# Kernel tuning notes

Measured on AMD Instinct MI355X. Metric: run time of the kernel, lower is better.

Reference implementation:

```python
import jax, jax.numpy as jnp
from jax import lax
import numpy as np

HID = 64      # lstm hidden / gat in-dim
HEADS = 4
DH = HID // HEADS  # 16 per-head dim
OUT = 3       # horizon


def setup_inputs() -> dict:
    key = jax.random.key(0)
    ks = jax.random.split(key, 18)
    B, T, N = 8, 12, 1500
    p = lambda k, shape: jax.random.normal(k, shape, jnp.float32) * 0.1
    return {
        "x": jax.random.normal(ks[0], (B, T, N), jnp.float32),
        "adj": jax.random.randint(ks[1], (N, N), 0, 2, jnp.int32),
        "lstm_Wih0": p(ks[2], (4 * HID, 1)),
        "lstm_Whh0": p(ks[3], (4 * HID, HID)),
        "lstm_bih0": p(ks[4], (4 * HID,)),
        "lstm_bhh0": p(ks[5], (4 * HID,)),
        "lstm_Wih1": p(ks[6], (4 * HID, HID)),
        "lstm_Whh1": p(ks[7], (4 * HID, HID)),
        "lstm_bih1": p(ks[8], (4 * HID,)),
        "lstm_bhh1": p(ks[9], (4 * HID,)),
        "gat0_W": p(ks[10], (HID, HID)),
        "gat0_asrc": p(ks[11], (HEADS, DH)),
        "gat0_adst": p(ks[12], (HEADS, DH)),
        "gat1_W": p(ks[13], (HID, HID)),
        "gat1_asrc": p(ks[14], (HEADS, DH)),
        "gat1_adst": p(ks[15], (HEADS, DH)),
        "out_W": p(ks[16], (OUT, HID)),
        "out_b": p(ks[17], (OUT,)),
    }


def _lstm_layer(seq, Wih, Whh, bih, bhh):
    # seq: (T, BN, in) -> (T, BN, H). PyTorch gate order i,f,g,o.
    BN = seq.shape[1]
    H = Whh.shape[1]

    def step(carry, xt):
        h, c = carry
        g = xt @ Wih.T + h @ Whh.T + bih + bhh
        i, f, gg, o = jnp.split(g, 4, axis=-1)
        c = jax.nn.sigmoid(f) * c + jax.nn.sigmoid(i) * jnp.tanh(gg)
        h = jax.nn.sigmoid(o) * jnp.tanh(c)
        return (h, c), h

    zero = jnp.zeros((BN, H), seq.dtype)
    _, hs = lax.scan(step, (zero, zero), seq)
    return hs


def _gat(h_in, W, asrc, adst, mask):
    # h_in: (B,N,HID); mask: (1,N,N,1) bool
    B, N, _ = h_in.shape
    Hn, D = asrc.shape
    hp = (h_in @ W.T).reshape(B, N, Hn, D)           # (B,N,H,D)
    e_src = jnp.einsum('bnhd,hd->bnh', hp, asrc)
    e_dst = jnp.einsum('bnhd,hd->bnh', hp, adst)
    e = e_src[:, :, None, :] + e_dst[:, None, :, :]   # (B,i,j,H)
    e = jnp.where(e > 0, e, 0.2 * e)                  # LeakyReLU(0.2)
    e = jnp.where(mask, e, -jnp.inf)
    alpha = jax.nn.softmax(e, axis=2)                 # softmax over neighbors j
    ho = jnp.einsum('bijh,bjhd->bihd', alpha, hp)
    return ho.reshape(B, N, Hn * D)


def reference(x, adj, lstm_Wih0, lstm_Whh0, lstm_bih0, lstm_bhh0,
              lstm_Wih1, lstm_Whh1, lstm_bih1, lstm_bhh1,
              gat0_W, gat0_asrc, gat0_adst, gat1_W, gat1_asrc, gat1_adst,
              out_W, out_b):
    B, T, N = x.shape
    # (B,T,N) -> (B*N, T, 1) -> time-major (T, B*N, 1)
    xf = jnp.transpose(x, (0, 2, 1)).reshape(B * N, T, 1)
    seq = jnp.transpose(xf, (1, 0, 2))
    hs = _lstm_layer(seq, lstm_Wih0, lstm_Whh0, lstm_bih0, lstm_bhh0)
    hs = _lstm_layer(hs, lstm_Wih1, lstm_Whh1, lstm_bih1, lstm_bhh1)
    h = hs[-1].reshape(B, N, HID)                     # last-step hidden of top layer
    mask = (adj > 0)[None, :, :, None]
    h = jax.nn.relu(_gat(h, gat0_W, gat0_asrc, gat0_adst, mask))
    h = jax.nn.relu(_gat(h, gat1_W, gat1_asrc, gat1_adst, mask))
    out = h @ out_W.T + out_b                         # (B,N,OUT)
    return jnp.transpose(out, (0, 2, 1))              # (B,OUT,N)
```

## Files before the change

kernel.cpp:

```cpp
#include <hip/hip_runtime.h>
#include <hip/hip_bf16.h>


#define BN 12000
#define NNODE 1500
#define NB 8
#define TT 12
#define NPAD 1536
#define LOG2E 1.44269504f

typedef __bf16 bf16x8 __attribute__((ext_vector_type(8)));
typedef __bf16 bf16x4 __attribute__((ext_vector_type(4)));
typedef float  f32x4  __attribute__((ext_vector_type(4)));

__device__ __forceinline__ float rcpf(float v) { return __builtin_amdgcn_rcpf(v); }
__device__ __forceinline__ float exp2f_(float v) { return __builtin_amdgcn_exp2f(v); }
__device__ __forceinline__ float sigf(float v) { return rcpf(1.f + __expf(-v)); }
__device__ __forceinline__ float tanhf_(float v) {
    return fmaf(2.f, rcpf(1.f + __expf(-2.f * v)), -1.f);
}

__device__ __forceinline__ bf16x8 ldcvt(const float* p) {
    f32x4 a = *(const f32x4*)p;
    f32x4 b = *(const f32x4*)(p + 4);
    bf16x8 r;
    #pragma unroll
    for (int i = 0; i < 4; ++i) { r[i] = (__bf16)a[i]; r[4 + i] = (__bf16)b[i]; }
    return r;
}

__global__ __launch_bounds__(512, 1) void lstm_mask_prep(
    const float* __restrict__ x,
    const float* __restrict__ Wih0, const float* __restrict__ Whh0,
    const float* __restrict__ bih0, const float* __restrict__ bhh0,
    const float* __restrict__ Wih1, const float* __restrict__ Whh1,
    const float* __restrict__ bih1, const float* __restrict__ bhh1,
    const int* __restrict__ adj, unsigned int* __restrict__ mask,
    const float* __restrict__ gW, const float* __restrict__ asrc,
    const float* __restrict__ adst,
    __bf16* __restrict__ hpT, float* __restrict__ esT, float* __restrict__ edT)
{
    if (blockIdx.x >= 750) {
        int wid  = (blockIdx.x - 750) * 8 + (threadIdx.x >> 6);
        int lane = threadIdx.x & 63;
        #pragma unroll 4
        for (int u = 0; u < 16; ++u) {
            int task = wid * 16 + u;
            int i = task / 24, ch = task - i * 24;
            int j = ch * 64 + lane;
            int a = (i < NNODE && j < NNODE) ? adj[i * NNODE + j] : 0;
            unsigned long long m = __ballot(a > 0);
            if (lane == 0 && i < 1504) *(unsigned long long*)&mask[i * 48 + ch * 2] = m;
        }
        return;
    }

    __shared__ __align__(16) __bf16 h0s[16 * 72];
    __shared__ __align__(16) __bf16 h1s[16 * 72];
    __shared__ __align__(16) float  xls[TT * 16];
    __shared__ float avs[128];
    __shared__ __align__(16) __bf16 hp_t[64 * 24];

    int tid  = threadIdx.x;
    int w    = __builtin_amdgcn_readfirstlane(tid >> 6);
    int lane = tid & 63;
    int l15  = lane & 15;
    int qd   = lane >> 4;
    bool lo  = l15 < 8;
    int dloc = l15 & 7;
    int d    = 8 * w + dloc;

    for (int e = tid; e < (16 * 72) / 2; e += 512) ((unsigned int*)h1s)[e] = 0u;
    if (tid < TT * 16) {
        int t = tid >> 4, m = tid & 15;
        int s = blockIdx.x * 16 + m;
        int bb = s / NNODE, nn = s - bb * NNODE;
        xls[tid] = x[bb * (TT * NNODE) + t * NNODE + nn];
    }
    if (tid < 64)       avs[tid] = asrc[tid] * LOG2E;
    else if (tid < 128) avs[tid] = adst[tid - 64] * LOG2E;

    int gA = (lo ? 0 : 64) + d;
    int gB = (lo ? 128 : 192) + d;
    bf16x8 B0A[2], B0B[2], B1A[4], B1B[4];
    #pragma unroll
    for (int kt = 0; kt < 2; ++kt) {
        B0A[kt] = ldcvt(&Whh0[gA * 64 + 32 * kt + 8 * qd]);
        B0B[kt] = ldcvt(&Whh0[gB * 64 + 32 * kt + 8 * qd]);
        B1A[kt] = ldcvt(&Wih1[gA * 64 + 32 * kt + 8 * qd]);
        B1B[kt] = ldcvt(&Wih1[gB * 64 + 32 * kt + 8 * qd]);
        B1A[kt + 2] = ldcvt(&Whh1[gA * 64 + 32 * kt + 8 * qd]);
        B1B[kt + 2] = ldcvt(&Whh1[gB * 64 + 32 * kt + 8 * qd]);
    }
    float b0A = bih0[gA] + bhh0[gA], b0B = bih0[gB] + bhh0[gB];
    float b1A = bih1[gA] + bhh1[gA], b1B = bih1[gB] + bhh1[gB];
    float w0A = Wih0[gA], w0B = Wih0[gB];

    float pwi = Wih0[d],       pbi = bih0[d]       + bhh0[d];
    float pwg = Wih0[128 + d], pbg = bih0[128 + d] + bhh0[128 + d];
    float pwo = Wih0[192 + d], pbo = bih0[192 + d] + bhh0[192 + d];

    float c0[2], c1[2];
    c0[0] = c0[1] = c1[0] = c1[1] = 0.f;

    __syncthreads();

    #pragma unroll
    for (int rl = 0; rl < 2; ++rl) {
        int rr = lo ? rl : 2 + rl;
        int m = 4 * qd + rr;
        float xv = xls[m];
        float gi = fmaf(pwi, xv, pbi);
        float gg = fmaf(pwg, xv, pbg);
        float go = fmaf(pwo, xv, pbo);
        float c = sigf(gi) * tanhf_(gg);
        c0[rl] = c;
        h0s[m * 72 + d] = (__bf16)(sigf(go) * tanhf_(c));
    }
    __syncthreads();

    for (int t = 0; t < TT; ++t) {
        bool last = (t == TT - 1);
        bf16x8 a0[2], a1[2];
        #pragma unroll
        for (int kt = 0; kt < 2; ++kt) {
            a0[kt] = *(bf16x8*)&h0s[l15 * 72 + 32 * kt + 8 * qd];
            a1[kt] = *(bf16x8*)&h1s[l15 * 72 + 32 * kt + 8 * qd];
        }
        f32x4 AA1, AB1, AA0, AB0;
        #pragma unroll
        for (int r = 0; r < 4; ++r) { AA1[r] = b1A; AB1[r] = b1B; }
        if (!last) {
            f32x4 xv = *(f32x4*)&xls[(t + 1) * 16 + 4 * qd];
            #pragma unroll
            for (int r = 0; r < 4; ++r) {
                AA0[r] = fmaf(w0A, xv[r], b0A);
                AB0[r] = fmaf(w0B, xv[r], b0B);
            }
        }
        #pragma unroll
        for (int kt = 0; kt < 2; ++kt) {
            AA1 = __builtin_amdgcn_mfma_f32_16x16x32_bf16(a0[kt], B1A[kt], AA1, 0, 0, 0);
            AB1 = __builtin_amdgcn_mfma_f32_16x16x32_bf16(a0[kt], B1B[kt], AB1, 0, 0, 0);
            AA1 = __builtin_amdgcn_mfma_f32_16x16x32_bf16(a1[kt], B1A[kt + 2], AA1, 0, 0, 0);
            AB1 = __builtin_amdgcn_mfma_f32_16x16x32_bf16(a1[kt], B1B[kt + 2], AB1, 0, 0, 0);
        }
        if (!last) {
            #pragma unroll
            for (int kt = 0; kt < 2; ++kt) {
                AA0 = __builtin_amdgcn_mfma_f32_16x16x32_bf16(a0[kt], B0A[kt], AA0, 0, 0, 0);
                AB0 = __builtin_amdgcn_mfma_f32_16x16x32_bf16(a0[kt], B0B[kt], AB0, 0, 0, 0);
            }
        }
        __syncthreads();

        {
            float shA0 = __shfl_xor(lo ? AA1[2] : AA1[0], 8);
            float shA1 = __shfl_xor(lo ? AA1[3] : AA1[1], 8);
            float shB0 = __shfl_xor(lo ? AB1[2] : AB1[0], 8);
            float shB1 = __shfl_xor(lo ? AB1[3] : AB1[1], 8);
            #pragma unroll
            for (int rl = 0; rl < 2; ++rl) {
                int rr = lo ? rl : 2 + rl;
                float ownA = AA1[rr], ownB = AB1[rr];
                float shA = rl ? shA1 : shA0, shB = rl ? shB1 : shB0;
                float gi = lo ? ownA : shA;
                float gf = lo ? shA : ownA;
                float gg = lo ? ownB : shB;
                float go = lo ? shB : ownB;
                float c = sigf(gf) * c1[rl] + sigf(gi) * tanhf_(gg);
                c1[rl] = c;
                float hv = sigf(go) * tanhf_(c);
                int m = 4 * qd + rr;
                h1s[m * 72 + d] = (__bf16)hv;
            }
        }
        if (!last) {
            float shA0 = __shfl_xor(lo ? AA0[2] : AA0[0], 8);
            float shA1 = __shfl_xor(lo ? AA0[3] : AA0[1], 8);
            float shB0 = __shfl_xor(lo ? AB0[2] : AB0[0], 8);
            float shB1 = __shfl_xor(lo ? AB0[3] : AB0[1], 8);
            #pragma unroll
            for (int rl = 0; rl < 2; ++rl) {
                int rr = lo ? rl : 2 + rl;
                float ownA = AA0[rr], ownB = AB0[rr];
                float shA = rl ? shA1 : shA0, shB = rl ? shB1 : shB0;
                float gi = lo ? ownA : shA;
                float gf = lo ? shA : ownA;
                float gg = lo ? ownB : shB;
                float go = lo ? shB : ownB;
                float c = sigf(gf) * c0[rl] + sigf(gi) * tanhf_(gg);
                c0[rl] = c;
                int m = 4 * qd + rr;
                h0s[m * 72 + d] = (__bf16)(sigf(go) * tanhf_(c));
            }
        }
        __syncthreads();
    }

    int s0 = blockIdx.x * 16;
    if (w < 4) {
        int mt = w;
        bf16x8 Bf0 = *(bf16x8*)&h1s[l15 * 72 + 8 * qd];
        bf16x8 Bf1 = *(bf16x8*)&h1s[l15 * 72 + 32 + 8 * qd];
        bf16x8 A0 = ldcvt(&gW[(mt * 16 + l15) * 64 + 8 * qd]);
        bf16x8 A1 = ldcvt(&gW[(mt * 16 + l15) * 64 + 32 + 8 * qd]);
        f32x4 a = {0.f, 0.f, 0.f, 0.f};
        a = __builtin_amdgcn_mfma_f32_16x16x32_bf16(A0, Bf0, a, 0, 0, 0);
        a = __builtin_amdgcn_mfma_f32_16x16x32_bf16(A1, Bf1, a, 0, 0, 0);
        float ts = 0.f, td = 0.f;
        #pragma unroll
        for (int r = 0; r < 4; ++r) {
            int dd = mt * 16 + qd * 4 + r;
            ts = fmaf(a[r], avs[dd], ts);
            td = fmaf(a[r], avs[64 + dd], td);
            hp_t[dd * 24 + l15] = (__bf16)a[r];
        }
        ts += __shfl_xor(ts, 16); ts += __shfl_xor(ts, 32);
        td += __shfl_xor(td, 16); td += __shfl_xor(td, 32);
        if (qd == 0) {
            int s = s0 + l15, b = s / NNODE, n = s - b * NNODE;
            esT[(b * 4 + mt) * NPAD + n] = ts;
            edT[(b * 4 + mt) * NPAD + n] = td;
        }
    }
    __syncthreads();
    if (tid < 256) {
        int dim = tid >> 2, seg = tid & 3;
        int b0 = s0 / NNODE, b1 = (s0 + 15) / NNODE;
        if (b0 == b1) {
            int n0 = s0 - b0 * NNODE;
            bf16x4 v = *(bf16x4*)&hp_t[dim * 24 + seg * 4];
            *(bf16x4*)&hpT[((b0 << 6) + dim) * NPAD + n0 + seg * 4] = v;
        } else {
            #pragma unroll
            for (int u = 0; u < 4; ++u) {
                int ss = s0 + seg * 4 + u;
                int b = ss / NNODE, n = ss - b * NNODE;
                hpT[((b << 6) + dim) * NPAD + n] = hp_t[dim * 24 + seg * 4 + u];
            }
        }
    }
}

__global__ __launch_bounds__(512, 1) void gat_mid(
    const __bf16* __restrict__ hpT, const float* __restrict__ esT,
    const float* __restrict__ edT, const unsigned int* __restrict__ mask,
    const float* __restrict__ gW, const float* __restrict__ asrc,
    const float* __restrict__ adst,
    __bf16* __restrict__ hpT1, float* __restrict__ esT1, float* __restrict__ edT1)
{
    __shared__ float Ss[8][16];
    __shared__ float hbuf[32 * 72];
    __shared__ float avs[128];
    __shared__ __align__(16) __bf16 hp1_t[64 * 40];

    int tid  = threadIdx.x;
    int wv   = tid >> 6;
    int lane = tid & 63;
    int l15  = lane & 15;
    int qd   = lane >> 4;
    int hh   = wv & 3;
    int ig   = wv >> 2;
    int b    = blockIdx.x / 47;
    int i0   = (blockIdx.x % 47) * 32;
    int it   = i0 + ig * 16;

    if (tid < 64)       avs[tid] = asrc[tid] * LOG2E;
    else if (tid < 128) avs[tid] = adst[tid - 64] * LOG2E;

    const __bf16* Brow = hpT + (((b << 6) + (hh << 4) + l15) * NPAD);
    const float* edrow = edT + (b * 4 + hh) * NPAD;
    const unsigned int* mrow = mask + (it + l15) * 48;
    float esv = esT[(b * 4 + hh) * NPAD + it + l15];

    f32x4 acc = {0.f, 0.f, 0.f, 0.f};
    float S = 0.f;

    for (int jt = 0; jt < 12; ++jt) {
        uint4 mw = *(const uint4*)&mrow[jt * 4];
        #pragma unroll
        for (int kt = 0; kt < 4; ++kt) {
            int jk = jt * 128 + kt * 32 + qd * 8;
            float4 e0 = *(const float4*)&edrow[jk];
            float4 e1 = *(const float4*)&edrow[jk + 4];
            unsigned int mb = ((&mw.x)[kt] >> (qd * 8)) & 0xffu;
            float ej[8] = {e0.x, e0.y, e0.z, e0.w, e1.x, e1.y, e1.z, e1.w};
            bf16x8 A;
            #pragma unroll
            for (int jj = 0; jj < 8; ++jj) {
                float e = esv + ej[jj];
                e = fmaxf(e, 0.2f * e);
                float p = ((mb >> jj) & 1u) ? exp2f_(e) : 0.f;
                S += p;
                A[jj] = (__bf16)p;
            }
            bf16x8 B = *(const bf16x8*)&Brow[jk];
            acc = __builtin_amdgcn_mfma_f32_16x16x32_bf16(A, B, acc, 0, 0, 0);
        }
    }

    S += __shfl_xor(S, 16);
    S += __shfl_xor(S, 32);
    if (qd == 0) Ss[wv][l15] = S;
    __syncthreads();

    #pragma unroll
    for (int r = 0; r < 4; ++r) {
        float rs = rcpf(Ss[wv][qd * 4 + r]);
        hbuf[(ig * 16 + qd * 4 + r) * 72 + (hh << 4) + l15] = fmaxf(acc[r] * rs, 0.f);
    }
    __syncthreads();

    {
        int mt = hh;
        bf16x8 Bf0 = ldcvt(&hbuf[(ig * 16 + l15) * 72 + 8 * qd]);
        bf16x8 Bf1 = ldcvt(&hbuf[(ig * 16 + l15) * 72 + 32 + 8 * qd]);
        bf16x8 A0 = ldcvt(&gW[(mt * 16 + l15) * 64 + 8 * qd]);
        bf16x8 A1 = ldcvt(&gW[(mt * 16 + l15) * 64 + 32 + 8 * qd]);
        f32x4 a = {0.f, 0.f, 0.f, 0.f};
        a = __builtin_amdgcn_mfma_f32_16x16x32_bf16(A0, Bf0, a, 0, 0, 0);
        a = __builtin_amdgcn_mfma_f32_16x16x32_bf16(A1, Bf1, a, 0, 0, 0);
        float ts = 0.f, td = 0.f;
        #pragma unroll
        for (int r = 0; r < 4; ++r) {
            int dd = mt * 16 + qd * 4 + r;
            ts = fmaf(a[r], avs[dd], ts);
            td = fmaf(a[r], avs[64 + dd], td);
            hp1_t[dd * 40 + ig * 16 + l15] = (__bf16)a[r];
        }
        ts += __shfl_xor(ts, 16); ts += __shfl_xor(ts, 32);
        td += __shfl_xor(td, 16); td += __shfl_xor(td, 32);
        if (qd == 0) {
            int n = i0 + ig * 16 + l15;
            esT1[(b * 4 + mt) * NPAD + n] = ts;
            edT1[(b * 4 + mt) * NPAD + n] = td;
        }
    }
    __syncthreads();
    if (tid < 256) {
        int dim = tid >> 2, seg = tid & 3;
        bf16x8 v = *(bf16x8*)&hp1_t[dim * 40 + seg * 8];
        *(bf16x8*)&hpT1[((b << 6) + dim) * NPAD + i0 + seg * 8] = v;
    }
}

__global__ __launch_bounds__(512, 1) void gat_fin(
    const __bf16* __restrict__ hpT, const float* __restrict__ esT,
    const float* __restrict__ edT, const unsigned int* __restrict__ mask,
    const float* __restrict__ oW, const float* __restrict__ ob,
    float* __restrict__ outp)
{
    __shared__ float Ss[8][16];
    __shared__ float hbuf[32 * 72];
    __shared__ float oWs[192];
    __shared__ float obs[3];

    int tid  = threadIdx.x;
    int wv   = tid >> 6;
    int lane = tid & 63;
    int l15  = lane & 15;
    int qd   = lane >> 4;
    int hh   = wv & 3;
    int ig   = wv >> 2;
    int b    = blockIdx.x / 47;
    int i0   = (blockIdx.x % 47) * 32;
    int it   = i0 + ig * 16;

    if (tid < 192) oWs[tid] = oW[tid];
    if (tid < 3)   obs[tid] = ob[tid];

    const __bf16* Brow = hpT + (((b << 6) + (hh << 4) + l15) * NPAD);
    const float* edrow = edT + (b * 4 + hh) * NPAD;
    const unsigned int* mrow = mask + (it + l15) * 48;
    float esv = esT[(b * 4 + hh) * NPAD + it + l15];

    f32x4 acc = {0.f, 0.f, 0.f, 0.f};
    float S = 0.f;

    for (int jt = 0; jt < 12; ++jt) {
        uint4 mw = *(const uint4*)&mrow[jt * 4];
        #pragma unroll
        for (int kt = 0; kt < 4; ++kt) {
            int jk = jt * 128 + kt * 32 + qd * 8;
            float4 e0 = *(const float4*)&edrow[jk];
            float4 e1 = *(const float4*)&edrow[jk + 4];
            unsigned int mb = ((&mw.x)[kt] >> (qd * 8)) & 0xffu;
            float ej[8] = {e0.x, e0.y, e0.z, e0.w, e1.x, e1.y, e1.z, e1.w};
            bf16x8 A;
            #pragma unroll
            for (int jj = 0; jj < 8; ++jj) {
                float e = esv + ej[jj];
                e = fmaxf(e, 0.2f * e);
                float p = ((mb >> jj) & 1u) ? exp2f_(e) : 0.f;
                S += p;
                A[jj] = (__bf16)p;
            }
            bf16x8 B = *(const bf16x8*)&Brow[jk];
            acc = __builtin_amdgcn_mfma_f32_16x16x32_bf16(A, B, acc, 0, 0, 0);
        }
    }

    S += __shfl_xor(S, 16);
    S += __shfl_xor(S, 32);
    if (qd == 0) Ss[wv][l15] = S;
    __syncthreads();

    #pragma unroll
    for (int r = 0; r < 4; ++r) {
        float rs = rcpf(Ss[wv][qd * 4 + r]);
        hbuf[(ig * 16 + qd * 4 + r) * 72 + (hh << 4) + l15] = fmaxf(acc[r] * rs, 0.f);
    }
    __syncthreads();

    if (tid < 384) {
        int idx = tid >> 2, ks = tid & 3;
        int nl = idx & 31, o = idx >> 5;
        if (i0 + nl < NNODE) {
            const float* hb = &hbuf[nl * 72 + ks * 16];
            float a = 0.f;
            #pragma unroll
            for (int kk = 0; kk < 16; ++kk)
                a = fmaf(hb[kk], oWs[o * 64 + ks * 16 + kk], a);
            a += __shfl_xor(a, 1);
            a += __shfl_xor(a, 2);
            if (ks == 0)
                outp[(long)b * 3 * NNODE + o * NNODE + i0 + nl] = a + obs[o];
        }
    }
}

extern "C" void kernel_launch(void* const* d_in, const int* in_sizes, int n_in,
                              void* d_out, int out_size, void* d_ws, size_t ws_size,
                              hipStream_t stream) {
    const float* x    = (const float*)d_in[0];
    const int*   adj  = (const int*)d_in[1];
    const float* Wih0 = (const float*)d_in[2];
    const float* Whh0 = (const float*)d_in[3];
    const float* bih0 = (const float*)d_in[4];
    const float* bhh0 = (const float*)d_in[5];
    const float* Wih1 = (const float*)d_in[6];
    const float* Whh1 = (const float*)d_in[7];
    const float* bih1 = (const float*)d_in[8];
    const float* bhh1 = (const float*)d_in[9];
    const float* g0W  = (const float*)d_in[10];
    const float* g0s  = (const float*)d_in[11];
    const float* g0d  = (const float*)d_in[12];
    const float* g1W  = (const float*)d_in[13];
    const float* g1s  = (const float*)d_in[14];
    const float* g1d  = (const float*)d_in[15];
    const float* oW   = (const float*)d_in[16];
    const float* ob   = (const float*)d_in[17];

    float* ws = (float*)d_ws;
    float*        esT0  = ws;
    float*        edT0  = ws + 49152;
    float*        esT1  = ws + 98304;
    float*        edT1  = ws + 147456;
    __bf16*       hpT0  = (__bf16*)(ws + 196608);
    __bf16*       hpT1  = (__bf16*)(ws + 589824);
    unsigned int* maskp = (unsigned int*)(ws + 983040);

    lstm_mask_prep<<<1032, 512, 0, stream>>>(x, Wih0, Whh0, bih0, bhh0,
                                             Wih1, Whh1, bih1, bhh1,
                                             adj, maskp, g0W, g0s, g0d,
                                             hpT0, esT0, edT0);
    gat_mid<<<376, 512, 0, stream>>>(hpT0, esT0, edT0, maskp,
                                     g1W, g1s, g1d, hpT1, esT1, edT1);
    gat_fin<<<376, 512, 0, stream>>>(hpT1, esT1, edT1, maskp,
                                     oW, ob, (float*)d_out);
}
```

Measured before the change: 219.5 us.

## Halve GAT block size and stage edst and mask tiles in LDS

The two GAT kernels now run 752 blocks of 256 threads, each covering 16 destination nodes with one wave per head, instead of 376 blocks of 512 threads covering 32 nodes. Each block first copies the batch's e_dst rows (4×NPAD floats) and a transposed 16-row mask tile into shared memory, so the inner loop reads them from LDS rather than global memory. The aim is more blocks to fill the CUs and cheaper inner-loop loads. In exchange, the e_dst staging is repeated per block with half as many nodes to share it, and each block uses more LDS.

```diff
diff --git a/kernel.cpp b/kernel.cpp
--- a/kernel.cpp
+++ b/kernel.cpp
@@ -243,48 +243,55 @@
     }
 }
 
-__global__ __launch_bounds__(512, 1) void gat_mid(
+__global__ __launch_bounds__(256, 1) void gat_mid(
     const __bf16* __restrict__ hpT, const float* __restrict__ esT,
     const float* __restrict__ edT, const unsigned int* __restrict__ mask,
     const float* __restrict__ gW, const float* __restrict__ asrc,
     const float* __restrict__ adst,
     __bf16* __restrict__ hpT1, float* __restrict__ esT1, float* __restrict__ edT1)
 {
-    __shared__ float Ss[8][16];
-    __shared__ float hbuf[32 * 72];
+    __shared__ __align__(16) float edls[4 * NPAD];
+    __shared__ unsigned int mskls[48 * 16];
+    __shared__ float Ss[4][16];
+    __shared__ float hbuf[16 * 72];
     __shared__ float avs[128];
-    __shared__ __align__(16) __bf16 hp1_t[64 * 40];
+    __shared__ __align__(16) __bf16 hp1_t[64 * 24];
 
     int tid  = threadIdx.x;
     int wv   = tid >> 6;
     int lane = tid & 63;
     int l15  = lane & 15;
     int qd   = lane >> 4;
-    int hh   = wv & 3;
-    int ig   = wv >> 2;
-    int b    = blockIdx.x / 47;
-    int i0   = (blockIdx.x % 47) * 32;
-    int it   = i0 + ig * 16;
+    int b    = blockIdx.x / 94;
+    int i0   = (blockIdx.x % 94) * 16;
 
     if (tid < 64)       avs[tid] = asrc[tid] * LOG2E;
     else if (tid < 128) avs[tid] = adst[tid - 64] * LOG2E;
-
-    const __bf16* Brow = hpT + (((b << 6) + (hh << 4) + l15) * NPAD);
-    const float* edrow = edT + (b * 4 + hh) * NPAD;
-    const unsigned int* mrow = mask + (it + l15) * 48;
-    float esv = esT[(b * 4 + hh) * NPAD + it + l15];
+    {
+        const float4* src = (const float4*)(edT + (b * 4) * NPAD);
+        float4* dst = (float4*)edls;
+        for (int u = tid; u < NPAD; u += 256) dst[u] = src[u];
+    }
+    for (int u = tid; u < 16 * 48; u += 256) {
+        int il = u / 48, c = u - il * 48;
+        mskls[c * 16 + il] = mask[(i0 + il) * 48 + c];
+    }
+    __syncthreads();
+
+    const __bf16* Brow = hpT + (((b << 6) + (wv << 4) + l15) * NPAD);
+    const float* edrow = edls + wv * NPAD;
+    float esv = esT[(b * 4 + wv) * NPAD + i0 + l15];
 
     f32x4 acc = {0.f, 0.f, 0.f, 0.f};
     float S = 0.f;
 
     for (int jt = 0; jt < 12; ++jt) {
-        uint4 mw = *(const uint4*)&mrow[jt * 4];
         #pragma unroll
         for (int kt = 0; kt < 4; ++kt) {
             int jk = jt * 128 + kt * 32 + qd * 8;
             float4 e0 = *(const float4*)&edrow[jk];
             float4 e1 = *(const float4*)&edrow[jk + 4];
-            unsigned int mb = ((&mw.x)[kt] >> (qd * 8)) & 0xffu;
+            unsigned int mb = (mskls[(jt * 4 + kt) * 16 + l15] >> (qd * 8)) & 0xffu;
             float ej[8] = {e0.x, e0.y, e0.z, e0.w, e1.x, e1.y, e1.z, e1.w};
             bf16x8 A;
             #pragma unroll
@@ -308,14 +315,14 @@
     #pragma unroll
     for (int r = 0; r < 4; ++r) {
         float rs = rcpf(Ss[wv][qd * 4 + r]);
-        hbuf[(ig * 16 + qd * 4 + r) * 72 + (hh << 4) + l15] = fmaxf(acc[r] * rs, 0.f);
+        hbuf[(qd * 4 + r) * 72 + (wv << 4) + l15] = fmaxf(acc[r] * rs, 0.f);
     }
     __syncthreads();
 
     {
-        int mt = hh;
-        bf16x8 Bf0 = ldcvt(&hbuf[(ig * 16 + l15) * 72 + 8 * qd]);
-        bf16x8 Bf1 = ldcvt(&hbuf[(ig * 16 + l15) * 72 + 32 + 8 * qd]);
+        int mt = wv;
+        bf16x8 Bf0 = ldcvt(&hbuf[l15 * 72 + 8 * qd]);
+        bf16x8 Bf1 = ldcvt(&hbuf[l15 * 72 + 32 + 8 * qd]);
         bf16x8 A0 = ldcvt(&gW[(mt * 16 + l15) * 64 + 8 * qd]);
         bf16x8 A1 = ldcvt(&gW[(mt * 16 + l15) * 64 + 32 + 8 * qd]);
         f32x4 a = {0.f, 0.f, 0.f, 0.f};
@@ -327,32 +334,34 @@
             int dd = mt * 16 + qd * 4 + r;
             ts = fmaf(a[r], avs[dd], ts);
             td = fmaf(a[r], avs[64 + dd], td);
-            hp1_t[dd * 40 + ig * 16 + l15] = (__bf16)a[r];
+            hp1_t[dd * 24 + l15] = (__bf16)a[r];
         }
         ts += __shfl_xor(ts, 16); ts += __shfl_xor(ts, 32);
         td += __shfl_xor(td, 16); td += __shfl_xor(td, 32);
         if (qd == 0) {
-            int n = i0 + ig * 16 + l15;
+            int n = i0 + l15;
             esT1[(b * 4 + mt) * NPAD + n] = ts;
             edT1[(b * 4 + mt) * NPAD + n] = td;
         }
     }
     __syncthreads();
-    if (tid < 256) {
+    {
         int dim = tid >> 2, seg = tid & 3;
-        bf16x8 v = *(bf16x8*)&hp1_t[dim * 40 + seg * 8];
-        *(bf16x8*)&hpT1[((b << 6) + dim) * NPAD + i0 + seg * 8] = v;
-    }
-}
-
-__global__ __launch_bounds__(512, 1) void gat_fin(
+        bf16x4 v = *(bf16x4*)&hp1_t[dim * 24 + seg * 4];
+        *(bf16x4*)&hpT1[((b << 6) + dim) * NPAD + i0 + seg * 4] = v;
+    }
+}
+
+__global__ __launch_bounds__(256, 1) void gat_fin(
     const __bf16* __restrict__ hpT, const float* __restrict__ esT,
     const float* __restrict__ edT, const unsigned int* __restrict__ mask,
     const float* __restrict__ oW, const float* __restrict__ ob,
     float* __restrict__ outp)
 {
-    __shared__ float Ss[8][16];
-    __shared__ float hbuf[32 * 72];
+    __shared__ __align__(16) float edls[4 * NPAD];
+    __shared__ unsigned int mskls[48 * 16];
+    __shared__ float Ss[4][16];
+    __shared__ float hbuf[16 * 72];
     __shared__ float oWs[192];
     __shared__ float obs[3];
 
@@ -361,31 +370,36 @@
     int lane = tid & 63;
     int l15  = lane & 15;
     int qd   = lane >> 4;
-    int hh   = wv & 3;
-    int ig   = wv >> 2;
-    int b    = blockIdx.x / 47;
-    int i0   = (blockIdx.x % 47) * 32;
-    int it   = i0 + ig * 16;
+    int b    = blockIdx.x / 94;
+    int i0   = (blockIdx.x % 94) * 16;
 
     if (tid < 192) oWs[tid] = oW[tid];
     if (tid < 3)   obs[tid] = ob[tid];
-
-    const __bf16* Brow = hpT + (((b << 6) + (hh << 4) + l15) * NPAD);
-    const float* edrow = edT + (b * 4 + hh) * NPAD;
-    const unsigned int* mrow = mask + (it + l15) * 48;
-    float esv = esT[(b * 4 + hh) * NPAD + it + l15];
+    {
+        const float4* src = (const float4*)(edT + (b * 4) * NPAD);
+        float4* dst = (float4*)edls;
+        for (int u = tid; u < NPAD; u += 256) dst[u] = src[u];
+    }
+    for (int u = tid; u < 16 * 48; u += 256) {
+        int il = u / 48, c = u - il * 48;
+        mskls[c * 16 + il] = mask[(i0 + il) * 48 + c];
+    }
+    __syncthreads();
+
+    const __bf16* Brow = hpT + (((b << 6) + (wv << 4) + l15) * NPAD);
+    const float* edrow = edls + wv * NPAD;
+    float esv = esT[(b * 4 + wv) * NPAD + i0 + l15];
 
     f32x4 acc = {0.f, 0.f, 0.f, 0.f};
     float S = 0.f;
 
     for (int jt = 0; jt < 12; ++jt) {
-        uint4 mw = *(const uint4*)&mrow[jt * 4];
         #pragma unroll
         for (int kt = 0; kt < 4; ++kt) {
             int jk = jt * 128 + kt * 32 + qd * 8;
             float4 e0 = *(const float4*)&edrow[jk];
             float4 e1 = *(const float4*)&edrow[jk + 4];
-            unsigned int mb = ((&mw.x)[kt] >> (qd * 8)) & 0xffu;
+            unsigned int mb = (mskls[(jt * 4 + kt) * 16 + l15] >> (qd * 8)) & 0xffu;
             float ej[8] = {e0.x, e0.y, e0.z, e0.w, e1.x, e1.y, e1.z, e1.w};
             bf16x8 A;
             #pragma unroll
@@ -409,13 +423,13 @@
     #pragma unroll
     for (int r = 0; r < 4; ++r) {
         float rs = rcpf(Ss[wv][qd * 4 + r]);
-        hbuf[(ig * 16 + qd * 4 + r) * 72 + (hh << 4) + l15] = fmaxf(acc[r] * rs, 0.f);
-    }
-    __syncthreads();
-
-    if (tid < 384) {
+        hbuf[(qd * 4 + r) * 72 + (wv << 4) + l15] = fmaxf(acc[r] * rs, 0.f);
+    }
+    __syncthreads();
+
+    if (tid < 192) {
         int idx = tid >> 2, ks = tid & 3;
-        int nl = idx & 31, o = idx >> 5;
+        int nl = idx & 15, o = idx >> 4;
         if (i0 + nl < NNODE) {
             const float* hb = &hbuf[nl * 72 + ks * 16];
             float a = 0.f;
@@ -465,8 +479,8 @@
                                              Wih1, Whh1, bih1, bhh1,
                                              adj, maskp, g0W, g0s, g0d,
                                              hpT0, esT0, edT0);
-    gat_mid<<<376, 512, 0, stream>>>(hpT0, esT0, edT0, maskp,
+    gat_mid<<<752, 256, 0, stream>>>(hpT0, esT0, edT0, maskp,
                                      g1W, g1s, g1d, hpT1, esT1, edT1);
-    gat_fin<<<376, 512, 0, stream>>>(hpT1, esT1, edT1, maskp,
+    gat_fin<<<752, 256, 0, stream>>>(hpT1, esT1, edT1, maskp,
                                      oW, ob, (float*)d_out);
 }
```

After: 190.8 us. 1.15x faster.
